# Performance work log

Measured on AMD Instinct MI355X. Metric: run time of the kernel, lower is better.

The kernel has to match this reference:

```python
import jax, jax.numpy as jnp
import numpy as np

N_NODES = 50000
N_REL = 8
N_EDGES = 100000
IN_SIZE = 128
OUT_SIZE = 128


def setup_inputs() -> dict:
    key = jax.random.key(0)
    k1, k2, k3, k4, k5 = jax.random.split(key, 5)
    inp = jax.random.normal(k1, (N_NODES, IN_SIZE), dtype=jnp.float32)
    src = jax.random.randint(k2, (N_REL, N_EDGES), 0, N_NODES, dtype=jnp.int32)
    dst = jax.random.randint(k3, (N_REL, N_EDGES), 0, N_NODES, dtype=jnp.int32)
    vals = jax.random.uniform(k4, (N_REL, N_EDGES), dtype=jnp.float32)
    weights = jax.random.normal(k5, (N_REL, IN_SIZE, OUT_SIZE), dtype=jnp.float32) * (1.0 / np.sqrt(IN_SIZE))
    return {"inp": inp, "src": src, "dst": dst, "vals": vals, "weights": weights}


def reference(inp, src, dst, vals, weights):
    # Per-relation sparse adj @ inp:  agg[r] = A_r @ inp, A_r given as COO edges.
    n_nodes = inp.shape[0]

    def rel_agg(s, d, v):
        msgs = v[:, None] * inp[s]                      # [E, in]
        return jax.ops.segment_sum(msgs, d, num_segments=n_nodes)  # [N, in]

    agg = jax.vmap(rel_agg)(src, dst, vals)             # [R, N, in]
    # concat along features then block-stacked weight matmul == per-relation
    # matmul summed over relations: out = sum_r agg[r] @ W[r]
    out = jnp.einsum('rni,rio->no', agg, weights)       # [N, out]
    return out
```

## Files before the change

### kernel.cpp

```cpp
#include <hip/hip_runtime.h>


constexpr int IN  = 128;
constexpr int OUT = 128;
constexpr int LDK = 136;
constexpr int NPB = 64;
constexpr int LDKB = 136;
constexpr int CAPMAX = 256;
constexpr int NBINS_MAX = 1024;
constexpr int EPB = 2048;

typedef __attribute__((ext_vector_type(8))) short bf16x8;
typedef __attribute__((ext_vector_type(4))) float f32x4;

__device__ inline unsigned short f2bf(float f) {
    unsigned int u = __float_as_uint(f);
    u += 0x7fffu + ((u >> 16) & 1u);
    return (unsigned short)(u >> 16);
}
__device__ inline float bflo(unsigned int u) { return __uint_as_float(u << 16); }
__device__ inline float bfhi(unsigned int u) { return __uint_as_float(u & 0xffff0000u); }
__device__ inline unsigned int pack2bf(float a, float b) {
    return (unsigned)f2bf(a) | ((unsigned)f2bf(b) << 16);
}
__device__ inline unsigned int cvtpk_bf16(float a, float b) {
    unsigned int r;
    asm("v_cvt_pk_bf16_f32 %0, %1, %2" : "=v"(r) : "v"(a), "v"(b));
    return r;
}

__global__ __launch_bounds__(256) void conv_inp_kernel(
    const float* __restrict__ x, unsigned short* __restrict__ y, int n8)
{
    const int i = blockIdx.x * 256 + threadIdx.x;
    if (i >= n8) return;
    const float4 a = ((const float4*)x)[i * 2];
    const float4 b = ((const float4*)x)[i * 2 + 1];
    uint4 o;
    o.x = pack2bf(a.x, a.y);
    o.y = pack2bf(a.z, a.w);
    o.z = pack2bf(b.x, b.y);
    o.w = pack2bf(b.z, b.w);
    ((uint4*)y)[i] = o;
}

__global__ __launch_bounds__(256) void conv_w_kernel(
    const float* __restrict__ w, unsigned short* __restrict__ wt, int total)
{
    const int t = blockIdx.x * 256 + threadIdx.x;
    if (t >= total) return;
    const int r = t >> 14, rem = t & 16383;
    const int n = rem >> 7, k = rem & 127;
    wt[t] = f2bf(w[(r << 14) + (k << 7) + n]);
}

__global__ __launch_bounds__(256) void prep_kernel(
    const int* __restrict__ src, const int* __restrict__ dst,
    const float* __restrict__ vals, int* __restrict__ bin_cnt,
    int2* __restrict__ binned, int4* __restrict__ spill,
    int* __restrict__ spill_cnt,
    int n_edges, int n_nodes, int nbins, int cap, int spill_max,
    int fgx, int nF,
    const float* __restrict__ x, unsigned short* __restrict__ y, int n8, int nbI,
    const float* __restrict__ w, unsigned short* __restrict__ wtb, int wtot)
{
    __shared__ int hist[NBINS_MAX];
    __shared__ int gbase[NBINS_MAX];

    const int bid = blockIdx.x;
    const int tid = threadIdx.x;

    if (bid >= nF) {
        const int cb = bid - nF;
        if (cb < nbI) {
            const int i = cb * 256 + tid;
            if (i >= n8) return;
            const float4 a = ((const float4*)x)[i * 2];
            const float4 b = ((const float4*)x)[i * 2 + 1];
            uint4 o;
            o.x = pack2bf(a.x, a.y);
            o.y = pack2bf(a.z, a.w);
            o.z = pack2bf(b.x, b.y);
            o.w = pack2bf(b.z, b.w);
            ((uint4*)y)[i] = o;
        } else {
            const int t = (cb - nbI) * 256 + tid;
            if (t >= wtot) return;
            const int r = t >> 14, rem = t & 16383;
            const int n = rem >> 7, k = rem & 127;
            wtb[t] = f2bf(w[(r << 14) + (k << 7) + n]);
        }
        return;
    }

    const int rel = bid / fgx;
    const int e0 = (bid - rel * fgx) * EPB;
    const size_t base_e = (size_t)rel * n_edges;

    for (int b = tid; b < nbins; b += 256) hist[b] = 0;
    __syncthreads();

    #pragma unroll
    for (int j = 0; j < EPB / 256; ++j) {
        const int e = e0 + j * 256 + tid;
        if (e < n_edges) atomicAdd(&hist[dst[base_e + e] >> 6], 1);
    }
    __syncthreads();

    for (int b = tid; b < nbins; b += 256) {
        const int c = hist[b];
        gbase[b] = c ? atomicAdd(&bin_cnt[rel * nbins + b], c) : 0;
        hist[b] = 0;
    }
    __syncthreads();

    #pragma unroll
    for (int j = 0; j < EPB / 256; ++j) {
        const int e = e0 + j * 256 + tid;
        if (e >= n_edges) continue;
        const int d = dst[base_e + e];
        const int s = src[base_e + e];
        const float v = vals[base_e + e];
        const int b = d >> 6;
        const int lp = atomicAdd(&hist[b], 1);
        const int pos = gbase[b] + lp;
        if (pos < cap) {
            binned[(size_t)(rel * nbins + b) * cap + pos] =
                make_int2(((d & 63) << 19) | s, __float_as_int(v));
        } else {
            const int sp = atomicAdd(spill_cnt, 1);
            if (sp < spill_max)
                spill[sp] = make_int4(d, (rel << 19) | s, __float_as_int(v), 0);
        }
    }
}

__global__ __launch_bounds__(256, 4) void bin_gemm_kernel(
    const unsigned short* __restrict__ inpb,
    const unsigned short* __restrict__ wt,
    const int2* __restrict__ binned, const int* __restrict__ bin_cnt,
    float* __restrict__ out, int n_nodes, int nbins, int cap, int n_rel)
{
    __shared__ unsigned short Ab[NPB * LDKB];
    __shared__ int2 sorted[CAPMAX];
    __shared__ int lcnt[NPB];
    __shared__ int loff[NPB + 1];
    __shared__ int lcur[NPB];
    __shared__ int relcnt[8];

    const int bin = blockIdx.x;
    const int tid = threadIdx.x;
    const int wave = tid >> 6, lane = tid & 63;
    const int m = lane & 15, q = lane >> 4;

    if (tid < n_rel) {
        int c = bin_cnt[tid * nbins + bin];
        relcnt[tid] = c > cap ? cap : c;
    }
    if (tid < NPB) { lcnt[tid] = 0; lcur[tid] = 0; }
    __syncthreads();

    int2 ecur = make_int2((NPB - 1) << 19, 0);
    if (tid < relcnt[0])
        ecur = binned[(size_t)bin * cap + tid];

    f32x4 acc[4][2];
    #pragma unroll
    for (int mt = 0; mt < 4; ++mt) {
        acc[mt][0] = (f32x4){0.f, 0.f, 0.f, 0.f};
        acc[mt][1] = (f32x4){0.f, 0.f, 0.f, 0.f};
    }

    for (int r = 0; r < n_rel; ++r) {
        const int cnt = relcnt[r];

        const unsigned short* wtr = wt + ((size_t)r * OUT + wave * 32) * IN;
        bf16x8 bfrag[2][4];
        #pragma unroll
        for (int nt = 0; nt < 2; ++nt)
            #pragma unroll
            for (int ks = 0; ks < 4; ++ks)
                bfrag[nt][ks] = *(const bf16x8*)(
                    wtr + (size_t)(nt * 16 + m) * IN + ks * 32 + q * 8);

        {
            uint4* A4 = (uint4*)Ab;
            #pragma unroll
            for (int j = 0; j < (NPB * LDKB / 8 + 255) / 256; ++j) {
                const int idx = j * 256 + tid;
                if (idx < NPB * LDKB / 8)
                    A4[idx] = make_uint4(0u, 0u, 0u, 0u);
            }
        }
        if (tid < cnt) atomicAdd(&lcnt[(ecur.x >> 19) & (NPB - 1)], 1);
        __syncthreads();

        if (tid < NPB) {
            const int v = lcnt[tid];
            int incl = v;
            #pragma unroll
            for (int off = 1; off < NPB; off <<= 1) {
                const int t = __shfl_up(incl, off, NPB);
                if (tid >= off) incl += t;
            }
            loff[tid] = incl - v;
            if (tid == NPB - 1) loff[NPB] = incl;
        }
        __syncthreads();

        if (tid < cnt) {
            const int g = (ecur.x >> 19) & (NPB - 1);
            const int pos = atomicAdd(&lcur[g], 1);
            sorted[loff[g] + pos] = ecur;
        }
        if (tid < NPB) lcnt[tid] = 0;
        __syncthreads();

        int2 enext = make_int2((NPB - 1) << 19, 0);
        if (r + 1 < n_rel && tid < relcnt[r + 1])
            enext = binned[(size_t)((r + 1) * nbins + bin) * cap + tid];

        {
            const int g0 = wave * 16;
            const int gend = g0 + 15;
            const int start = loff[g0];
            const int end = loff[g0 + 16];
            int cur = g0;
            float a0 = 0.f, a1 = 0.f;
            for (int i = start; i < end; i += 8) {
                int2 e[8]; unsigned int u[8];
                #pragma unroll
                for (int k = 0; k < 8; ++k) {
                    const int idx = i + k;
                    e[k] = (idx < end) ? sorted[idx]
                                       : make_int2(gend << 19, 0);
                }
                #pragma unroll
                for (int k = 0; k < 8; ++k)
                    u[k] = ((const unsigned int*)(
                        inpb + (size_t)(e[k].x & 0x7ffff) * IN))[lane];
                #pragma unroll
                for (int k = 0; k < 8; ++k) {
                    const int ln = (e[k].x >> 19) & (NPB - 1);
                    if (ln != cur) {
                        *(unsigned int*)&Ab[cur * LDKB + lane * 2] =
                            cvtpk_bf16(a0, a1);
                        a0 = 0.f; a1 = 0.f; cur = ln;
                    }
                    const float v = __int_as_float(e[k].y);
                    a0 += v * bflo(u[k]); a1 += v * bfhi(u[k]);
                }
            }
            *(unsigned int*)&Ab[cur * LDKB + lane * 2] = cvtpk_bf16(a0, a1);
        }
        if (tid < NPB) lcur[tid] = 0;
        __syncthreads();

        #pragma unroll
        for (int ks = 0; ks < 4; ++ks) {
            bf16x8 a[4];
            #pragma unroll
            for (int mt = 0; mt < 4; ++mt)
                a[mt] = *(const bf16x8*)&Ab[(mt * 16 + m) * LDKB
                                            + ks * 32 + q * 8];
            #pragma unroll
            for (int mt = 0; mt < 4; ++mt) {
                acc[mt][0] = __builtin_amdgcn_mfma_f32_16x16x32_bf16(
                    a[mt], bfrag[0][ks], acc[mt][0], 0, 0, 0);
                acc[mt][1] = __builtin_amdgcn_mfma_f32_16x16x32_bf16(
                    a[mt], bfrag[1][ks], acc[mt][1], 0, 0, 0);
            }
        }
        ecur = enext;
        __syncthreads();
    }

    const int row0 = bin * NPB;
    #pragma unroll
    for (int mt = 0; mt < 4; ++mt) {
        #pragma unroll
        for (int rg = 0; rg < 4; ++rg) {
            const int row = row0 + mt * 16 + q * 4 + rg;
            if (row < n_nodes) {
                float* op = out + (size_t)row * OUT + wave * 32 + m;
                op[0]  = acc[mt][0][rg];
                op[16] = acc[mt][1][rg];
            }
        }
    }
}

__global__ __launch_bounds__(256) void spill_w_kernel(
    const unsigned short* __restrict__ inpb,
    const unsigned short* __restrict__ wt,
    const int4* __restrict__ spill, const int* __restrict__ spill_cnt,
    float* __restrict__ out, int spill_max)
{
    int n = *spill_cnt;
    if (n > spill_max) n = spill_max;
    const int w = (blockIdx.x * 256 + threadIdx.x) >> 6;
    const int lane = threadIdx.x & 63;
    const int nw = gridDim.x * 4;
    for (int i = w; i < n; i += nw) {
        const int4 s = spill[i];
        const int d = s.x;
        const int rel = s.y >> 19, srcrow = s.y & 0x7ffff;
        const float v = __int_as_float(s.z);
        const unsigned short* irow = inpb + (size_t)srcrow * IN;
        #pragma unroll
        for (int cc = 0; cc < 2; ++cc) {
            const int col = lane * 2 + cc;
            const unsigned short* wrow = wt + ((size_t)rel * OUT + col) * IN;
            float acc = 0.f;
            for (int k8 = 0; k8 < IN; k8 += 8) {
                const uint4 iw = *(const uint4*)(irow + k8);
                const uint4 ww = *(const uint4*)(wrow + k8);
                acc += bflo(iw.x)*bflo(ww.x) + bfhi(iw.x)*bfhi(ww.x)
                     + bflo(iw.y)*bflo(ww.y) + bfhi(iw.y)*bfhi(ww.y)
                     + bflo(iw.z)*bflo(ww.z) + bfhi(iw.z)*bfhi(ww.z)
                     + bflo(iw.w)*bflo(ww.w) + bfhi(iw.w)*bfhi(ww.w);
            }
            __hip_atomic_fetch_add(out + (size_t)d * OUT + col, v * acc,
                                   __ATOMIC_RELAXED, __HIP_MEMORY_SCOPE_AGENT);
        }
    }
}

__global__ __launch_bounds__(256) void mfma_gemm(
    const unsigned short* __restrict__ inpb,
    const unsigned short* __restrict__ wt,
    unsigned short* __restrict__ h, int rel_base, int n_nodes)
{
    __shared__ unsigned short As[128 * LDK];

    const int rel = rel_base + blockIdx.y;
    const int row0 = blockIdx.x * 128;
    const int tid = threadIdx.x;
    const int wave = tid >> 6, lane = tid & 63;
    const int m = lane & 15, q = lane >> 4;

    {
        const int r = tid >> 1;
        const int half = (tid & 1) * 64;
        const int grow = row0 + r;
        const uint4* gp = (const uint4*)(inpb + (size_t)grow * IN + half);
        uint4* lp = (uint4*)&As[r * LDK + half];
        #pragma unroll
        for (int i = 0; i < 8; ++i) {
            uint4 v = make_uint4(0u, 0u, 0u, 0u);
            if (grow < n_nodes) v = gp[i];
            lp[i] = v;
        }
    }

    bf16x8 bfrag[2][4];
    {
        const unsigned short* wtr = wt + ((size_t)rel * OUT + wave * 32) * IN;
        #pragma unroll
        for (int nt = 0; nt < 2; ++nt)
            #pragma unroll
            for (int ks = 0; ks < 4; ++ks)
                bfrag[nt][ks] = *(const bf16x8*)(
                    wtr + (size_t)(nt * 16 + m) * IN + ks * 32 + q * 8);
    }

    __syncthreads();

    f32x4 acc[8][2];
    #pragma unroll
    for (int mt = 0; mt < 8; ++mt)
        #pragma unroll
        for (int nt = 0; nt < 2; ++nt)
            acc[mt][nt] = (f32x4){0.f, 0.f, 0.f, 0.f};

    #pragma unroll
    for (int ks = 0; ks < 4; ++ks) {
        bf16x8 a[8];
        #pragma unroll
        for (int mt = 0; mt < 8; ++mt)
            a[mt] = *(const bf16x8*)&As[(mt * 16 + m) * LDK + ks * 32 + q * 8];
        #pragma unroll
        for (int mt = 0; mt < 8; ++mt) {
            acc[mt][0] = __builtin_amdgcn_mfma_f32_16x16x32_bf16(
                a[mt], bfrag[0][ks], acc[mt][0], 0, 0, 0);
            acc[mt][1] = __builtin_amdgcn_mfma_f32_16x16x32_bf16(
                a[mt], bfrag[1][ks], acc[mt][1], 0, 0, 0);
        }
    }

    unsigned short* hrel = h + (size_t)blockIdx.y * n_nodes * OUT;
    #pragma unroll
    for (int mt = 0; mt < 8; ++mt) {
        #pragma unroll
        for (int rg = 0; rg < 4; ++rg) {
            const int row = row0 + mt * 16 + q * 4 + rg;
            if (row < n_nodes) {
                unsigned short* hp = hrel + (size_t)row * OUT + wave * 32 + m;
                hp[0]  = f2bf(acc[mt][0][rg]);
                hp[16] = f2bf(acc[mt][1][rg]);
            }
        }
    }
}

__global__ __launch_bounds__(256) void fill_kernel(
    const int* __restrict__ src, const int* __restrict__ dst,
    const float* __restrict__ vals, int* __restrict__ counts,
    int2* __restrict__ bucket, int4* __restrict__ spill,
    int* __restrict__ spill_cnt, int n_edges, int n_nodes,
    int cap, int spill_max)
{
    const int e = blockIdx.x * 256 + threadIdx.x;
    if (e >= n_edges) return;
    const size_t g = (size_t)blockIdx.y * n_edges + e;
    const int d = dst[g];
    const int enc = blockIdx.y * n_nodes + src[g];
    const int pos = atomicAdd(&counts[d], 1);
    if (pos < cap) {
        bucket[(size_t)d * cap + pos] = make_int2(enc, __float_as_int(vals[g]));
    } else {
        const int sp = atomicAdd(spill_cnt, 1);
        if (sp < spill_max)
            spill[sp] = make_int4(d, enc, __float_as_int(vals[g]), 0);
    }
}

__global__ __launch_bounds__(256) void gather_kernel(
    const unsigned short* __restrict__ h, const int2* __restrict__ bucket,
    const int* __restrict__ counts, float* __restrict__ out,
    int n_nodes, int cap, int accum)
{
    const int node = blockIdx.x * 8 + (threadIdx.x >> 5);
    const int lane = threadIdx.x & 31;
    if (node >= n_nodes) return;
    int cnt = counts[node];
    if (cnt > cap) cnt = cap;
    const int2* __restrict__ b = bucket + (size_t)node * cap;
    float4* __restrict__ op = (float4*)(out + (size_t)node * OUT);

    float4 acc = accum ? op[lane] : make_float4(0.f, 0.f, 0.f, 0.f);
    int j = 0;
    for (; j + 4 <= cnt; j += 4) {
        const int2 r0 = b[j], r1 = b[j + 1], r2 = b[j + 2], r3 = b[j + 3];
        const uint2 h0 = ((const uint2*)(h + (size_t)r0.x * OUT))[lane];
        const uint2 h1 = ((const uint2*)(h + (size_t)r1.x * OUT))[lane];
        const uint2 h2 = ((const uint2*)(h + (size_t)r2.x * OUT))[lane];
        const uint2 h3 = ((const uint2*)(h + (size_t)r3.x * OUT))[lane];
        const float v0 = __int_as_float(r0.y), v1 = __int_as_float(r1.y);
        const float v2 = __int_as_float(r2.y), v3 = __int_as_float(r3.y);
        acc.x += v0*bflo(h0.x) + v1*bflo(h1.x) + v2*bflo(h2.x) + v3*bflo(h3.x);
        acc.y += v0*bfhi(h0.x) + v1*bfhi(h1.x) + v2*bfhi(h2.x) + v3*bfhi(h3.x);
        acc.z += v0*bflo(h0.y) + v1*bflo(h1.y) + v2*bflo(h2.y) + v3*bflo(h3.y);
        acc.w += v0*bfhi(h0.y) + v1*bfhi(h1.y) + v2*bfhi(h2.y) + v3*bfhi(h3.y);
    }
    for (; j < cnt; ++j) {
        const int2 r0 = b[j];
        const float v = __int_as_float(r0.y);
        const uint2 hv = ((const uint2*)(h + (size_t)r0.x * OUT))[lane];
        acc.x += v * bflo(hv.x); acc.y += v * bfhi(hv.x);
        acc.z += v * bflo(hv.y); acc.w += v * bfhi(hv.y);
    }
    op[lane] = acc;
}

__global__ __launch_bounds__(256) void spill_kernel(
    const unsigned short* __restrict__ h, const int4* __restrict__ spill,
    const int* __restrict__ spill_cnt, float* __restrict__ out, int spill_max)
{
    int n = *spill_cnt;
    if (n > spill_max) n = spill_max;
    const int w = (blockIdx.x * 256 + threadIdx.x) >> 6;
    const int lane = threadIdx.x & 63;
    const int nw = gridDim.x * 4;
    for (int i = w; i < n; i += nw) {
        const int4 s = spill[i];
        const float v = __int_as_float(s.z);
        const unsigned int u = ((const unsigned int*)(h + (size_t)s.y * OUT))[lane];
        float* __restrict__ orow = out + (size_t)s.x * OUT;
        __hip_atomic_fetch_add(orow + lane * 2,     v * bflo(u),
                               __ATOMIC_RELAXED, __HIP_MEMORY_SCOPE_AGENT);
        __hip_atomic_fetch_add(orow + lane * 2 + 1, v * bfhi(u),
                               __ATOMIC_RELAXED, __HIP_MEMORY_SCOPE_AGENT);
    }
}

__global__ __launch_bounds__(256) void scatter_kernel(
    const unsigned short* __restrict__ h, const int* __restrict__ src,
    const int* __restrict__ dst, const float* __restrict__ vals,
    float* __restrict__ out, int n_edges)
{
    const int e = blockIdx.x * 8 + (threadIdx.x >> 5);
    if (e >= n_edges) return;
    const int lane = threadIdx.x & 31;
    const int s = src[e];
    const int d = dst[e];
    const float v = vals[e];
    const unsigned int* __restrict__ hrow =
        (const unsigned int*)(h + (size_t)s * OUT);
    float* __restrict__ orow = out + (size_t)d * OUT;
    #pragma unroll
    for (int kk = 0; kk < 2; ++kk) {
        const int jj = lane + kk * 32;
        const unsigned int u = hrow[jj];
        __hip_atomic_fetch_add(orow + jj * 2,     v * bflo(u),
                               __ATOMIC_RELAXED, __HIP_MEMORY_SCOPE_AGENT);
        __hip_atomic_fetch_add(orow + jj * 2 + 1, v * bfhi(u),
                               __ATOMIC_RELAXED, __HIP_MEMORY_SCOPE_AGENT);
    }
}

extern "C" void kernel_launch(void* const* d_in, const int* in_sizes, int n_in,
                              void* d_out, int out_size, void* d_ws, size_t ws_size,
                              hipStream_t stream) {
    const float* inp     = (const float*)d_in[0];
    const int*   src     = (const int*)  d_in[1];
    const int*   dst     = (const int*)  d_in[2];
    const float* vals    = (const float*)d_in[3];
    const float* weights = (const float*)d_in[4];
    float* out = (float*)d_out;

    const int n_nodes = in_sizes[0] / IN;
    const int n_rel   = in_sizes[4] / (IN * OUT);
    const int n_edges = in_sizes[1] / n_rel;

    auto align_up = [](size_t x) { return (x + 255) & ~(size_t)255; };
    const int SPILL_MAX = 65536;
    const size_t sz_inpb   = align_up((size_t)n_nodes * IN * 2);
    const size_t sz_wt     = align_up((size_t)n_rel * IN * OUT * 2);
    const size_t sz_spill  = align_up((size_t)SPILL_MAX * 16);

    const int conv_n8 = n_nodes * IN / 8;
    const int wt_tot  = n_rel * IN * OUT;
    const int gemm_gx = (n_nodes + 127) / 128;
    const int gath_gx = (n_nodes + 7) / 8;
    const int fill_gx = (n_edges + 255) / 256;
    const int nbins   = (n_nodes + NPB - 1) / NPB;

    if (n_rel <= 8 && n_nodes < (1 << 19) && nbins <= NBINS_MAX) {
        const size_t ncells  = (size_t)n_rel * nbins;
        const size_t sz_bcnt = align_up((ncells + 1) * 4);
        int cap = 0;
        const int caps[] = {256, 192, 128};
        for (int c : caps) {
            const size_t sz_binned = align_up(ncells * c * 8);
            if (sz_inpb + sz_wt + sz_bcnt + sz_spill + sz_binned <= ws_size) {
                cap = c; break;
            }
        }
        if (cap > 0) {
            const size_t sz_binned = align_up(ncells * cap * 8);
            char* p = (char*)d_ws;
            unsigned short* inpb = (unsigned short*)p;  p += sz_inpb;
            unsigned short* wtb  = (unsigned short*)p;  p += sz_wt;
            int*   bin_cnt = (int*)p;   p += sz_bcnt;
            int4*  spill   = (int4*)p;  p += sz_spill;
            int2*  binned  = (int2*)p;  p += sz_binned;
            int*   spill_cnt = bin_cnt + ncells;

            const int nbI = (conv_n8 + 255) / 256;
            const int nbW = (wt_tot + 255) / 256;
            const int fgx = (n_edges + EPB - 1) / EPB;
            const int nF  = fgx * n_rel;

            hipMemsetAsync(bin_cnt, 0, (ncells + 1) * 4, stream);
            prep_kernel<<<nF + nbI + nbW, 256, 0, stream>>>(
                src, dst, vals, bin_cnt, binned, spill, spill_cnt,
                n_edges, n_nodes, nbins, cap, SPILL_MAX, fgx, nF,
                inp, inpb, conv_n8, nbI, weights, wtb, wt_tot);
            bin_gemm_kernel<<<nbins, 256, 0, stream>>>(
                inpb, wtb, binned, bin_cnt, out, n_nodes, nbins, cap, n_rel);
            spill_w_kernel<<<128, 256, 0, stream>>>(
                inpb, wtb, spill, spill_cnt, out, SPILL_MAX);
            return;
        }
    }

    const size_t sz_counts = align_up((size_t)(n_nodes + 1) * 4);
    const size_t fixed = sz_inpb + sz_wt + sz_counts + sz_spill;

    {
        const size_t sz_h = (size_t)n_rel * n_nodes * OUT * 2;
        int cap = 0;
        const int caps[] = {64, 48, 32, 24, 20};
        for (int c : caps) {
            if (fixed + sz_h + align_up((size_t)n_nodes * c * 8) <= ws_size) {
                cap = c; break;
            }
        }
        if (cap > 0) {
            char* p = (char*)d_ws;
            unsigned short* inpb = (unsigned short*)p;  p += sz_inpb;
            unsigned short* wtb  = (unsigned short*)p;  p += sz_wt;
            int*   counts = (int*)p;    p += sz_counts;
            int4*  spill  = (int4*)p;   p += sz_spill;
            unsigned short* h = (unsigned short*)p;     p += sz_h;
            int2*  bucket = (int2*)p;
            int*   spill_cnt = counts + n_nodes;

            conv_inp_kernel<<<(conv_n8 + 255) / 256, 256, 0, stream>>>(
                inp, inpb, conv_n8);
            conv_w_kernel<<<(wt_tot + 255) / 256, 256, 0, stream>>>(
                weights, wtb, wt_tot);
            hipMemsetAsync(counts, 0, (size_t)(n_nodes + 1) * 4, stream);
            dim3 fg(fill_gx, n_rel);
            fill_kernel<<<fg, 256, 0, stream>>>(src, dst, vals, counts, bucket,
                                                spill, spill_cnt, n_edges,
                                                n_nodes, cap, SPILL_MAX);
            dim3 gg(gemm_gx, n_rel);
            mfma_gemm<<<gg, 256, 0, stream>>>(inpb, wtb, h, 0, n_nodes);
            gather_kernel<<<gath_gx, 256, 0, stream>>>(h, bucket, counts, out,
                                                       n_nodes, cap, 0);
            spill_kernel<<<128, 256, 0, stream>>>(h, spill, spill_cnt, out,
                                                  SPILL_MAX);
            return;
        }
    }

    {
        char* p = (char*)d_ws;
        unsigned short* inpb = (unsigned short*)p;  p += sz_inpb;
        unsigned short* wtb  = (unsigned short*)p;  p += sz_wt;
        unsigned short* h = (unsigned short*)p;

        conv_inp_kernel<<<(conv_n8 + 255) / 256, 256, 0, stream>>>(
            inp, inpb, conv_n8);
        conv_w_kernel<<<(wt_tot + 255) / 256, 256, 0, stream>>>(
            weights, wtb, wt_tot);
        hipMemsetAsync(out, 0, (size_t)n_nodes * OUT * 4, stream);
        const int sgx = (n_edges + 7) / 8;
        for (int r = 0; r < n_rel; ++r) {
            const size_t eoff = (size_t)r * n_edges;
            dim3 gg(gemm_gx, 1);
            mfma_gemm<<<gg, 256, 0, stream>>>(inpb, wtb, h, r, n_nodes);
            scatter_kernel<<<sgx, 256, 0, stream>>>(h, src + eoff, dst + eoff,
                                                    vals + eoff, out, n_edges);
        }
    }
}
```

Measured before the change: 185.5 us.

## Sort all relations' edges once per bin upfront and deepen gather unroll

The per-relation counting sort in shared memory is replaced by a single upfront sort over all relations' edges for the bin, using 512 groups (relation × local node). The per-relation loop therefore loses two barriers and the atomic/scan phases. Only the Ab rows with no edges are zeroed, instead of the whole tile. The gather unroll depth goes from 8 to 16 to keep more loads in flight. In exchange, shared memory and register use rise, and launch bounds are lowered to 3 blocks per SM, which reduces occupancy.

```diff
diff --git a/kernel.cpp b/kernel.cpp
--- a/kernel.cpp
+++ b/kernel.cpp
@@ -6,7 +6,9 @@
 constexpr int LDK = 136;
 constexpr int NPB = 64;
 constexpr int LDKB = 136;
-constexpr int CAPMAX = 256;
+constexpr int NG = 512;
+constexpr int MAXS = 2048;
+constexpr int DEPTH = 16;
 constexpr int NBINS_MAX = 1024;
 constexpr int EPB = 2048;
 
@@ -135,34 +137,85 @@
     }
 }
 
-__global__ __launch_bounds__(256, 4) void bin_gemm_kernel(
+__global__ __launch_bounds__(256, 3) void bin_gemm_kernel(
     const unsigned short* __restrict__ inpb,
     const unsigned short* __restrict__ wt,
     const int2* __restrict__ binned, const int* __restrict__ bin_cnt,
     float* __restrict__ out, int n_nodes, int nbins, int cap, int n_rel)
 {
     __shared__ unsigned short Ab[NPB * LDKB];
-    __shared__ int2 sorted[CAPMAX];
-    __shared__ int lcnt[NPB];
-    __shared__ int loff[NPB + 1];
-    __shared__ int lcur[NPB];
-    __shared__ int relcnt[8];
+    __shared__ int2 sorted[MAXS];
+    __shared__ int lcnt[NG];
+    __shared__ int loff[NG + 1];
+    __shared__ int lcur[NG];
+    __shared__ int coff[9];
 
     const int bin = blockIdx.x;
     const int tid = threadIdx.x;
     const int wave = tid >> 6, lane = tid & 63;
     const int m = lane & 15, q = lane >> 4;
 
-    if (tid < n_rel) {
-        int c = bin_cnt[tid * nbins + bin];
-        relcnt[tid] = c > cap ? cap : c;
-    }
-    if (tid < NPB) { lcnt[tid] = 0; lcur[tid] = 0; }
-    __syncthreads();
-
-    int2 ecur = make_int2((NPB - 1) << 19, 0);
-    if (tid < relcnt[0])
-        ecur = binned[(size_t)bin * cap + tid];
+    for (int i = tid; i < NG; i += 256) { lcnt[i] = 0; lcur[i] = 0; }
+    if (tid == 0) {
+        int s = 0; coff[0] = 0;
+        for (int r = 0; r < 8; ++r) {
+            int c = (r < n_rel) ? bin_cnt[r * nbins + bin] : 0;
+            if (c > cap) c = cap;
+            s += c; coff[r + 1] = s;
+        }
+    }
+    __syncthreads();
+
+    int co[9];
+    #pragma unroll
+    for (int j = 0; j < 9; ++j) co[j] = coff[j];
+    const int T = co[8];
+
+    int2 ereg[8]; int grp[8];
+    #pragma unroll
+    for (int k = 0; k < 8; ++k) {
+        const int idx = tid + k * 256;
+        int2 e = make_int2(0, 0); int g = -1;
+        if (idx < T) {
+            int c = 0;
+            #pragma unroll
+            for (int j = 1; j < 8; ++j) c += (idx >= co[j]);
+            const int pos = idx - co[c];
+            e = binned[(size_t)(c * nbins + bin) * cap + pos];
+            g = c * 64 + ((e.x >> 19) & 63);
+        }
+        ereg[k] = e; grp[k] = g;
+    }
+    #pragma unroll
+    for (int k = 0; k < 8; ++k)
+        if (grp[k] >= 0) atomicAdd(&lcnt[grp[k]], 1);
+    __syncthreads();
+
+    if (tid < 64) {
+        const int base = tid * 8;
+        int v[8]; int s = 0;
+        #pragma unroll
+        for (int i = 0; i < 8; ++i) { v[i] = s; s += lcnt[base + i]; }
+        int incl = s;
+        #pragma unroll
+        for (int off = 1; off < 64; off <<= 1) {
+            const int t = __shfl_up(incl, off, 64);
+            if (tid >= off) incl += t;
+        }
+        const int excl = incl - s;
+        #pragma unroll
+        for (int i = 0; i < 8; ++i) loff[base + i] = excl + v[i];
+        if (tid == 63) loff[NG] = incl;
+    }
+    __syncthreads();
+
+    #pragma unroll
+    for (int k = 0; k < 8; ++k)
+        if (grp[k] >= 0) {
+            const int pos = atomicAdd(&lcur[grp[k]], 1);
+            sorted[loff[grp[k]] + pos] = ereg[k];
+        }
+    __syncthreads();
 
     f32x4 acc[4][2];
     #pragma unroll
@@ -172,7 +225,7 @@
     }
 
     for (int r = 0; r < n_rel; ++r) {
-        const int cnt = relcnt[r];
+        const int gbase = r * 64;
 
         const unsigned short* wtr = wt + ((size_t)r * OUT + wave * 32) * IN;
         bf16x8 bfrag[2][4];
@@ -183,65 +236,38 @@
                 bfrag[nt][ks] = *(const bf16x8*)(
                     wtr + (size_t)(nt * 16 + m) * IN + ks * 32 + q * 8);
 
+        if (tid < NPB) {
+            if (loff[gbase + tid] == loff[gbase + tid + 1]) {
+                uint4* zp = (uint4*)&Ab[tid * LDKB];
+                #pragma unroll
+                for (int i = 0; i < 16; ++i)
+                    zp[i] = make_uint4(0u, 0u, 0u, 0u);
+            }
+        }
+
         {
-            uint4* A4 = (uint4*)Ab;
-            #pragma unroll
-            for (int j = 0; j < (NPB * LDKB / 8 + 255) / 256; ++j) {
-                const int idx = j * 256 + tid;
-                if (idx < NPB * LDKB / 8)
-                    A4[idx] = make_uint4(0u, 0u, 0u, 0u);
-            }
-        }
-        if (tid < cnt) atomicAdd(&lcnt[(ecur.x >> 19) & (NPB - 1)], 1);
-        __syncthreads();
-
-        if (tid < NPB) {
-            const int v = lcnt[tid];
-            int incl = v;
-            #pragma unroll
-            for (int off = 1; off < NPB; off <<= 1) {
-                const int t = __shfl_up(incl, off, NPB);
-                if (tid >= off) incl += t;
-            }
-            loff[tid] = incl - v;
-            if (tid == NPB - 1) loff[NPB] = incl;
-        }
-        __syncthreads();
-
-        if (tid < cnt) {
-            const int g = (ecur.x >> 19) & (NPB - 1);
-            const int pos = atomicAdd(&lcur[g], 1);
-            sorted[loff[g] + pos] = ecur;
-        }
-        if (tid < NPB) lcnt[tid] = 0;
-        __syncthreads();
-
-        int2 enext = make_int2((NPB - 1) << 19, 0);
-        if (r + 1 < n_rel && tid < relcnt[r + 1])
-            enext = binned[(size_t)((r + 1) * nbins + bin) * cap + tid];
-
-        {
-            const int g0 = wave * 16;
-            const int gend = g0 + 15;
+            const int g0 = gbase + wave * 16;
             const int start = loff[g0];
             const int end = loff[g0 + 16];
-            int cur = g0;
+            const int lnbase = wave * 16;
+            const int gend = lnbase + 15;
+            int cur = lnbase;
             float a0 = 0.f, a1 = 0.f;
-            for (int i = start; i < end; i += 8) {
-                int2 e[8]; unsigned int u[8];
+            for (int i = start; i < end; i += DEPTH) {
+                int2 e[DEPTH]; unsigned int u[DEPTH];
                 #pragma unroll
-                for (int k = 0; k < 8; ++k) {
+                for (int k = 0; k < DEPTH; ++k) {
                     const int idx = i + k;
                     e[k] = (idx < end) ? sorted[idx]
                                        : make_int2(gend << 19, 0);
                 }
                 #pragma unroll
-                for (int k = 0; k < 8; ++k)
+                for (int k = 0; k < DEPTH; ++k)
                     u[k] = ((const unsigned int*)(
                         inpb + (size_t)(e[k].x & 0x7ffff) * IN))[lane];
                 #pragma unroll
-                for (int k = 0; k < 8; ++k) {
-                    const int ln = (e[k].x >> 19) & (NPB - 1);
+                for (int k = 0; k < DEPTH; ++k) {
+                    const int ln = (e[k].x >> 19) & 63;
                     if (ln != cur) {
                         *(unsigned int*)&Ab[cur * LDKB + lane * 2] =
                             cvtpk_bf16(a0, a1);
@@ -253,7 +279,6 @@
             }
             *(unsigned int*)&Ab[cur * LDKB + lane * 2] = cvtpk_bf16(a0, a1);
         }
-        if (tid < NPB) lcur[tid] = 0;
         __syncthreads();
 
         #pragma unroll
@@ -271,7 +296,6 @@
                     a[mt], bfrag[1][ks], acc[mt][1], 0, 0, 0);
             }
         }
-        ecur = enext;
         __syncthreads();
     }
 
```

Result: slower. 212.0 us (+14.3%).
